# Kernel tuning notes

Hardware: AMD Instinct MI355X
Metric: run time of the kernel (lower is better)

The kernel has to match this reference:

```python
import jax, jax.numpy as jnp
import numpy as np

B, T, XD, ZD, H = 1024, 1000, 8, 8, 256


def setup_inputs() -> dict:
    key = jax.random.key(0)
    ks = jax.random.split(key, 10)
    # monotonically increasing time grid, identical per batch element: [B, T, 1]
    t = jnp.broadcast_to(jnp.linspace(0.0, 10.0, T, dtype=jnp.float32)[None, :, None], (B, T, 1))
    x = jax.random.normal(ks[0], (B, T, XD), jnp.float32)
    z = jax.random.normal(ks[1], (B, T, ZD), jnp.float32)
    event_t = jax.random.uniform(ks[2], (B, 1), jnp.float32, 3.0, 7.0)
    z_jump = jax.random.normal(ks[3], (B, ZD), jnp.float32)
    in_dim = 3 * (XD + ZD)

    def lin(k, fan_in, fan_out):
        return jax.random.normal(k, (fan_in, fan_out), jnp.float32) * (1.0 / np.sqrt(fan_in))

    W1 = lin(ks[4], in_dim, H); b1 = jnp.zeros((H,), jnp.float32)
    W2 = lin(ks[5], H, H);     b2 = jnp.zeros((H,), jnp.float32)
    W3 = lin(ks[6], H, H);     b3 = jnp.zeros((H,), jnp.float32)
    W4 = lin(ks[7], H, XD);    b4 = jnp.zeros((XD,), jnp.float32)
    return dict(t=t, x=x, z=z, event_t=event_t, z_jump=z_jump,
                W1=W1, b1=b1, W2=W2, b2=b2, W3=W3, b3=b3, W4=W4, b4=b4)


def reference(t, x, z, event_t, z_jump, W1, b1, W2, b2, W3, b3, W4, b4):
    # all_initial = cat(x[:,0], z[:,0]) : [B, XD+ZD]
    all_initial = jnp.concatenate([x[:, 0], z[:, 0]], axis=-1)

    def de_func(x_cur, z_eff):
        xtzt = jnp.concatenate([x_cur, z_eff], axis=-1)                      # [B, XD+ZD]
        inp = jnp.concatenate([all_initial, xtzt - all_initial, xtzt], -1)   # [B, 3*(XD+ZD)]
        h = jax.nn.elu(inp @ W1 + b1)
        h = jax.nn.elu(h @ W2 + b2)
        h = jax.nn.elu(h @ W3 + b3)
        return h @ W4 + b4                                                   # [B, XD]

    t_seq = jnp.moveaxis(t, 1, 0)   # [T, B, 1]
    z_seq = jnp.moveaxis(z, 1, 0)   # [T, B, ZD]
    dt = t_seq[1:] - t_seq[:-1]     # [T-1, B, 1]

    def step(x_cur, step_in):
        t_i, dt_i, z_i = step_in
        # event: once t passes event_t, exogenous z jumps to z_jump
        z_eff = jnp.where(t_i >= event_t, z_jump, z_i)
        x_next = x_cur + dt_i * de_func(x_cur, z_eff)  # explicit Euler step
        return x_next, x_next

    x0 = x[:, 0]  # initial condition [B, XD]
    _, xs = jax.lax.scan(step, x0, (t_seq[:-1], dt, z_seq[:-1]))
    sol = jnp.concatenate([x0[None], xs], axis=0)  # [T, B, XD]
    return jnp.moveaxis(sol, 0, 1)                 # [B, T, XD]
```

## Files before the change

kernel.cpp:

```cpp
#include <hip/hip_runtime.h>
#include <cstdint>
#include <cstddef>

typedef __bf16 bf16x8 __attribute__((ext_vector_type(8)));
typedef float f32x4 __attribute__((ext_vector_type(4)));

#define HD 256
#define TLEN 1000
#define NSTEP 999

#define W1R_OFF 0
#define W2R_OFF 16384
#define W3R_OFF 81920
#define W4R_OFF 147456
#define WS_ELEMS 151552

__device__ __forceinline__ void wg_barrier() {
  asm volatile("s_waitcnt lgkmcnt(0)\n\ts_barrier" ::: "memory");
}

__global__ void prep_weights(const float* __restrict__ W1, const float* __restrict__ b1,
                             const float* __restrict__ W2, const float* __restrict__ W3,
                             const float* __restrict__ W4, __bf16* __restrict__ ws) {
  int tid = blockIdx.x * blockDim.x + threadIdx.x;
  if (tid >= WS_ELEMS) return;
  float val = 0.0f;
  if (tid < W2R_OFF) {
    int t = tid;
    int j = t & 7, lane = (t >> 3) & 63, tt = (t >> 9) & 1, kb = (t >> 10) & 1, w = (t >> 11) & 7;
    int k = kb * 32 + ((lane >> 4) * 8) + j;
    int n = w * 32 + tt * 16 + (lane & 15);
    if (k < 48) val = W1[k * HD + n];
    else if (k == 48) val = b1[n];
  } else if (tid < W3R_OFF) {
    int t = tid - W2R_OFF;
    int j = t & 7, lane = (t >> 3) & 63, tt = (t >> 9) & 1, kb = (t >> 10) & 7, w = (t >> 13) & 7;
    int k = kb * 32 + ((lane >> 4) * 8) + j;
    int n = w * 32 + tt * 16 + (lane & 15);
    val = W2[k * HD + n];
  } else if (tid < W4R_OFF) {
    int t = tid - W3R_OFF;
    int j = t & 7, lane = (t >> 3) & 63, tt = (t >> 9) & 1, kb = (t >> 10) & 7, w = (t >> 13) & 7;
    int k = kb * 32 + ((lane >> 4) * 8) + j;
    int n = w * 32 + tt * 16 + (lane & 15);
    val = W3[k * HD + n];
  } else {
    int t = tid - W4R_OFF;
    int j = t & 7, lane = (t >> 3) & 63, kb = (t >> 9) & 7;
    int k = kb * 32 + ((lane >> 4) * 8) + j;
    int n = lane & 15;
    val = (n < 8) ? W4[k * 8 + n] : 0.0f;
  }
  ws[tid] = (__bf16)val;
}

__global__ __launch_bounds__(512, 2) void ode_main(
    const float* __restrict__ t_g, const float* __restrict__ x_g,
    const float* __restrict__ z_g, const float* __restrict__ ev_g,
    const float* __restrict__ zj_g, const float* __restrict__ b2_g,
    const float* __restrict__ b3_g, const float* __restrict__ b4_g,
    const __bf16* __restrict__ ws, float* __restrict__ out) {
  __shared__ __align__(16) __bf16 h_a[16 * 264];
  __shared__ __align__(16) __bf16 h_b[16 * 264];
  __shared__ __align__(16) float p4[8 * 16 * 8];
  __shared__ __align__(16) float x_cur[16 * 12];
  __shared__ __align__(16) float z_eff[16 * 12];
  __shared__ __align__(16) float x0s[16 * 12];
  __shared__ __align__(16) float z0s[16 * 12];
  __shared__ __align__(16) float zjs[16 * 12];
  __shared__ float evs[16];

  const int tid  = threadIdx.x;
  const int lane = tid & 63;
  const int wid  = tid >> 6;
  const int bcol = lane & 15;
  const int q    = lane >> 4;
  const int b0   = blockIdx.x * 8;

  if (tid < 128) {
    int m = tid >> 3, d = tid & 7;
    if (m < 8) {
      size_t gb = (size_t)(b0 + m);
      float x0 = x_g[gb * (TLEN * 8) + d];
      float z0 = z_g[gb * (TLEN * 8) + d];
      x0s[m * 12 + d] = x0;
      z0s[m * 12 + d] = z0;
      x_cur[m * 12 + d] = x0;
      zjs[m * 12 + d] = zj_g[gb * 8 + d];
      out[gb * (TLEN * 8) + d] = x0;
      if (d == 0) evs[m] = ev_g[gb];
    } else {
      x0s[m * 12 + d] = 0.f;
      z0s[m * 12 + d] = 0.f;
      x_cur[m * 12 + d] = 0.f;
      zjs[m * 12 + d] = 0.f;
      if (d == 0) evs[m] = 0.f;
    }
  }
  __syncthreads();

  if (tid < 128) {
    int m = tid >> 3, d = tid & 7;
    float t0 = t_g[0];
    z_eff[m * 12 + d] = (t0 >= evs[m]) ? zjs[m * 12 + d] : z0s[m * 12 + d];
  }

  const bf16x8* wsv = (const bf16x8*)ws;
  bf16x8 w1f[2][2], w2f[8][2], w3f[8][2];
#pragma unroll
  for (int kb = 0; kb < 2; ++kb)
#pragma unroll
    for (int tt = 0; tt < 2; ++tt)
      w1f[kb][tt] = wsv[(W1R_OFF / 8) + ((wid * 2 + kb) * 2 + tt) * 64 + lane];
#pragma unroll
  for (int kb = 0; kb < 8; ++kb)
#pragma unroll
    for (int tt = 0; tt < 2; ++tt) {
      w2f[kb][tt] = wsv[(W2R_OFF / 8) + ((wid * 8 + kb) * 2 + tt) * 64 + lane];
      w3f[kb][tt] = wsv[(W3R_OFF / 8) + ((wid * 8 + kb) * 2 + tt) * 64 + lane];
    }
  bf16x8 w4f = wsv[(W4R_OFF / 8) + wid * 64 + lane];

  f32x4 b2v[2], b3v[2];
#pragma unroll
  for (int tt = 0; tt < 2; ++tt) {
    int n0 = wid * 32 + tt * 16 + q * 4;
    b2v[tt] = *(const f32x4*)(b2_g + n0);
    b3v[tt] = *(const f32x4*)(b3_g + n0);
  }
  float b4l = (tid < 64) ? b4_g[tid & 7] : 0.0f;

  const int m1 = lane >> 2;
  const int d0 = (lane & 3) * 2;
  float2 zjf = make_float2(0.f, 0.f);
  float ev1 = 0.f;
  const bool zprod = (wid == 2) && (lane < 32);
  if (zprod) {
    zjf.x = zjs[m1 * 12 + d0];
    zjf.y = zjs[m1 * 12 + d0 + 1];
    ev1 = evs[m1];
  }

  f32x4 sub0, sub1;
  bf16x8 a0c;
  {
    const float* base = ((q & 1) ? z0s : x0s) + bcol * 12;
    f32x4 r0 = *(const f32x4*)(base);
    f32x4 r1 = *(const f32x4*)(base + 4);
    sub0 = r0; sub1 = r1;
#pragma unroll
    for (int e = 0; e < 4; ++e) { a0c[e] = (__bf16)r0[e]; a0c[e + 4] = (__bf16)r1[e]; }
  }
  bf16x8 zf;
#pragma unroll
  for (int e = 0; e < 8; ++e) zf[e] = (__bf16)0.f;
  bf16x8 k48f = zf;
  k48f[0] = (__bf16)1.0f;

  __syncthreads();

  float tc = t_g[0];

  auto layer = [&](const __bf16* src, __bf16* dst, const bf16x8 (*wf)[2], const f32x4* bv) {
    bf16x8 bfr[8];
    const bf16x8* hp = (const bf16x8*)src;
#pragma unroll
    for (int kb = 0; kb < 8; ++kb) bfr[kb] = hp[bcol * 33 + kb * 4 + q];
#pragma unroll
    for (int tt = 0; tt < 2; ++tt) {
      f32x4 c = bv[tt];
#pragma unroll
      for (int kb = 0; kb < 8; ++kb)
        c = __builtin_amdgcn_mfma_f32_16x16x32_bf16(wf[kb][tt], bfr[kb], c, 0, 0, 0);
      union { __bf16 h4[4]; unsigned long long u; } pk;
#pragma unroll
      for (int e = 0; e < 4; ++e) {
        float v = c[e];
        v = (v > 0.f) ? v : (__expf(v) - 1.0f);
        pk.h4[e] = (__bf16)v;
      }
      *(unsigned long long*)(dst + bcol * 264 + wid * 32 + tt * 16 + q * 4) = pk.u;
    }
  };

#pragma unroll 1
  for (int i = 0; i < NSTEP; ++i) {
    float tn = t_g[i + 1];
    float2 zpre = make_float2(0.f, 0.f);
    if (zprod)
      zpre = *(const float2*)(z_g + ((size_t)(b0 + m1) * TLEN + (i + 1)) * 8 + d0);

    {
      const float* rp = ((q & 1) ? z_eff : x_cur) + bcol * 12;
      f32x4 r0 = *(const f32x4*)(rp);
      f32x4 r1 = *(const f32x4*)(rp + 4);
      bf16x8 f0, f1;
      if (q < 2) {
        f0 = a0c;
#pragma unroll
        for (int e = 0; e < 4; ++e) { f1[e] = (__bf16)r0[e]; f1[e + 4] = (__bf16)r1[e]; }
      } else {
#pragma unroll
        for (int e = 0; e < 4; ++e) {
          f0[e] = (__bf16)(r0[e] - sub0[e]);
          f0[e + 4] = (__bf16)(r1[e] - sub1[e]);
        }
        f1 = (q == 2) ? k48f : zf;
      }
#pragma unroll
      for (int tt = 0; tt < 2; ++tt) {
        f32x4 c = {0.f, 0.f, 0.f, 0.f};
        c = __builtin_amdgcn_mfma_f32_16x16x32_bf16(w1f[0][tt], f0, c, 0, 0, 0);
        c = __builtin_amdgcn_mfma_f32_16x16x32_bf16(w1f[1][tt], f1, c, 0, 0, 0);
        union { __bf16 h4[4]; unsigned long long u; } pk;
#pragma unroll
        for (int e = 0; e < 4; ++e) {
          float v = c[e];
          v = (v > 0.f) ? v : (__expf(v) - 1.0f);
          pk.h4[e] = (__bf16)v;
        }
        *(unsigned long long*)(h_a + bcol * 264 + wid * 32 + tt * 16 + q * 4) = pk.u;
      }
    }
    wg_barrier();
    layer(h_a, h_b, w2f, b2v);
    wg_barrier();
    layer(h_b, h_a, w3f, b3v);

    {
      const bf16x8* hp = (const bf16x8*)h_a;
      bf16x8 h4 = hp[bcol * 33 + wid * 4 + q];
      f32x4 c = {0.f, 0.f, 0.f, 0.f};
      c = __builtin_amdgcn_mfma_f32_16x16x32_bf16(w4f, h4, c, 0, 0, 0);
      if (q < 2)
        *(f32x4*)(p4 + wid * 128 + bcol * 8 + q * 4) = c;
    }
    wg_barrier();

    float dt = tn - tc;
    if (tid < 64) {
      int m = tid >> 3, d = tid & 7;
      float s = b4l;
#pragma unroll
      for (int j = 0; j < 8; ++j) s += p4[j * 128 + m * 8 + d];
      float xn = x_cur[m * 12 + d] + dt * s;
      x_cur[m * 12 + d] = xn;
      out[(size_t)(b0 + m) * (TLEN * 8) + (size_t)(i + 1) * 8 + d] = xn;
    } else if (zprod) {
      bool jmp = (tn >= ev1);
      float2 zev = make_float2(jmp ? zjf.x : zpre.x, jmp ? zjf.y : zpre.y);
      *(float2*)(z_eff + m1 * 12 + d0) = zev;
    }
    tc = tn;
    wg_barrier();
  }
}

extern "C" void kernel_launch(void* const* d_in, const int* in_sizes, int n_in,
                              void* d_out, int out_size, void* d_ws, size_t ws_size,
                              hipStream_t stream) {
  const float* t  = (const float*)d_in[0];
  const float* x  = (const float*)d_in[1];
  const float* z  = (const float*)d_in[2];
  const float* ev = (const float*)d_in[3];
  const float* zj = (const float*)d_in[4];
  const float* W1 = (const float*)d_in[5];
  const float* b1 = (const float*)d_in[6];
  const float* W2 = (const float*)d_in[7];
  const float* b2 = (const float*)d_in[8];
  const float* W3 = (const float*)d_in[9];
  const float* b3 = (const float*)d_in[10];
  const float* W4 = (const float*)d_in[11];
  const float* b4 = (const float*)d_in[12];
  __bf16* ws = (__bf16*)d_ws;
  float* out = (float*)d_out;

  prep_weights<<<592, 256, 0, stream>>>(W1, b1, W2, W3, W4, ws);
  ode_main<<<128, 512, 0, stream>>>(t, x, z, ev, zj, b2, b3, b4, ws, out);
}
```

Before: 1.764 ms.

## Fold constant W1 terms into per-block init and compute output layer redundantly per wave

Rewrites layer 1 algebraically: the all_initial and bias contributions are precomputed once into a per-wave accumulator, and the per-step input shrinks to a single K=32 MFMA per tile using combined W1 rows. Every wave now computes the full layer-4 output itself, with a full K reduction held in registers, so the p4 shared reduction is gone. The x and z state lives in registers, which removes one barrier per step. Layer 2/3 accumulation is split into two independent MFMA chains to shorten the dependency chain. In exchange, each wave does redundant layer-4 MFMAs, holds extra weight registers, and uses a third LDS buffer.

New measurement: 2.024 ms. 1.15x slower.

```diff
diff --git a/kernel.cpp b/kernel.cpp
--- a/kernel.cpp
+++ b/kernel.cpp
@@ -9,7 +9,8 @@
 #define TLEN 1000
 #define NSTEP 999
 
-#define W1R_OFF 0
+#define W1X_OFF 0
+#define W1C_OFF 8192
 #define W2R_OFF 16384
 #define W3R_OFF 81920
 #define W4R_OFF 147456
@@ -25,13 +26,28 @@
   int tid = blockIdx.x * blockDim.x + threadIdx.x;
   if (tid >= WS_ELEMS) return;
   float val = 0.0f;
-  if (tid < W2R_OFF) {
+  if (tid < W1C_OFF) {
     int t = tid;
-    int j = t & 7, lane = (t >> 3) & 63, tt = (t >> 9) & 1, kb = (t >> 10) & 1, w = (t >> 11) & 7;
-    int k = kb * 32 + ((lane >> 4) * 8) + j;
-    int n = w * 32 + tt * 16 + (lane & 15);
-    if (k < 48) val = W1[k * HD + n];
-    else if (k == 48) val = b1[n];
+    int j = t & 7, lane = (t >> 3) & 63, tt = (t >> 9) & 1, w = (t >> 10) & 7;
+    int q = lane >> 4;
+    int n = w * 32 + tt * 16 + (lane & 15);
+    if (j < 4) {
+      int d = q * 4 + j;
+      if (q < 2) val = W1[(16 + d) * HD + n] + W1[(32 + d) * HD + n];
+      else { int dz = d - 8; val = W1[(24 + dz) * HD + n] + W1[(40 + dz) * HD + n]; }
+    }
+  } else if (tid < W2R_OFF) {
+    int t = tid - W1C_OFF;
+    int j = t & 7, lane = (t >> 3) & 63, tt = (t >> 9) & 1, w = (t >> 10) & 7;
+    int q = lane >> 4;
+    int n = w * 32 + tt * 16 + (lane & 15);
+    if (j < 4) {
+      int d = q * 4 + j;
+      if (q < 2) val = W1[d * HD + n] - W1[(16 + d) * HD + n];
+      else { int dz = d - 8; val = W1[(8 + dz) * HD + n] - W1[(24 + dz) * HD + n]; }
+    } else if (q == 0 && j == 4) {
+      val = b1[n];
+    }
   } else if (tid < W3R_OFF) {
     int t = tid - W2R_OFF;
     int j = t & 7, lane = (t >> 3) & 63, tt = (t >> 9) & 1, kb = (t >> 10) & 7, w = (t >> 13) & 7;
@@ -39,7 +55,8 @@
     int n = w * 32 + tt * 16 + (lane & 15);
     val = W2[k * HD + n];
   } else if (tid < W4R_OFF) {
-    int t = tid - W3R_OFF;
+    int t = tid - W4R_OFF + (W4R_OFF - W3R_OFF);
+    t = tid - W3R_OFF;
     int j = t & 7, lane = (t >> 3) & 63, tt = (t >> 9) & 1, kb = (t >> 10) & 7, w = (t >> 13) & 7;
     int k = kb * 32 + ((lane >> 4) * 8) + j;
     int n = w * 32 + tt * 16 + (lane & 15);
@@ -60,15 +77,9 @@
     const float* __restrict__ zj_g, const float* __restrict__ b2_g,
     const float* __restrict__ b3_g, const float* __restrict__ b4_g,
     const __bf16* __restrict__ ws, float* __restrict__ out) {
-  __shared__ __align__(16) __bf16 h_a[16 * 264];
-  __shared__ __align__(16) __bf16 h_b[16 * 264];
-  __shared__ __align__(16) float p4[8 * 16 * 8];
-  __shared__ __align__(16) float x_cur[16 * 12];
-  __shared__ __align__(16) float z_eff[16 * 12];
-  __shared__ __align__(16) float x0s[16 * 12];
-  __shared__ __align__(16) float z0s[16 * 12];
-  __shared__ __align__(16) float zjs[16 * 12];
-  __shared__ float evs[16];
+  __shared__ __align__(16) __bf16 hA[16 * 264];
+  __shared__ __align__(16) __bf16 hB[16 * 264];
+  __shared__ __align__(16) __bf16 hC[16 * 264];
 
   const int tid  = threadIdx.x;
   const int lane = tid & 63;
@@ -76,50 +87,23 @@
   const int bcol = lane & 15;
   const int q    = lane >> 4;
   const int b0   = blockIdx.x * 8;
-
-  if (tid < 128) {
-    int m = tid >> 3, d = tid & 7;
-    if (m < 8) {
-      size_t gb = (size_t)(b0 + m);
-      float x0 = x_g[gb * (TLEN * 8) + d];
-      float z0 = z_g[gb * (TLEN * 8) + d];
-      x0s[m * 12 + d] = x0;
-      z0s[m * 12 + d] = z0;
-      x_cur[m * 12 + d] = x0;
-      zjs[m * 12 + d] = zj_g[gb * 8 + d];
-      out[gb * (TLEN * 8) + d] = x0;
-      if (d == 0) evs[m] = ev_g[gb];
-    } else {
-      x0s[m * 12 + d] = 0.f;
-      z0s[m * 12 + d] = 0.f;
-      x_cur[m * 12 + d] = 0.f;
-      zjs[m * 12 + d] = 0.f;
-      if (d == 0) evs[m] = 0.f;
-    }
-  }
-  __syncthreads();
-
-  if (tid < 128) {
-    int m = tid >> 3, d = tid & 7;
-    float t0 = t_g[0];
-    z_eff[m * 12 + d] = (t0 >= evs[m]) ? zjs[m * 12 + d] : z0s[m * 12 + d];
-  }
+  const bool live = bcol < 8;
+  const size_t gb = (size_t)(b0 + (live ? bcol : 0));
 
   const bf16x8* wsv = (const bf16x8*)ws;
-  bf16x8 w1f[2][2], w2f[8][2], w3f[8][2];
-#pragma unroll
-  for (int kb = 0; kb < 2; ++kb)
-#pragma unroll
-    for (int tt = 0; tt < 2; ++tt)
-      w1f[kb][tt] = wsv[(W1R_OFF / 8) + ((wid * 2 + kb) * 2 + tt) * 64 + lane];
-#pragma unroll
-  for (int kb = 0; kb < 8; ++kb)
+  bf16x8 w1f[2], w2f[8][2], w3f[8][2], w4f[8];
+#pragma unroll
+  for (int tt = 0; tt < 2; ++tt)
+    w1f[tt] = wsv[(W1X_OFF / 8) + (wid * 2 + tt) * 64 + lane];
+#pragma unroll
+  for (int kb = 0; kb < 8; ++kb) {
 #pragma unroll
     for (int tt = 0; tt < 2; ++tt) {
       w2f[kb][tt] = wsv[(W2R_OFF / 8) + ((wid * 8 + kb) * 2 + tt) * 64 + lane];
       w3f[kb][tt] = wsv[(W3R_OFF / 8) + ((wid * 8 + kb) * 2 + tt) * 64 + lane];
     }
-  bf16x8 w4f = wsv[(W4R_OFF / 8) + wid * 64 + lane];
+    w4f[kb] = wsv[(W4R_OFF / 8) + kb * 64 + lane];
+  }
 
   f32x4 b2v[2], b3v[2];
 #pragma unroll
@@ -128,38 +112,62 @@
     b2v[tt] = *(const f32x4*)(b2_g + n0);
     b3v[tt] = *(const f32x4*)(b3_g + n0);
   }
-  float b4l = (tid < 64) ? b4_g[tid & 7] : 0.0f;
-
-  const int m1 = lane >> 2;
-  const int d0 = (lane & 3) * 2;
-  float2 zjf = make_float2(0.f, 0.f);
+  f32x4 b4v = {0.f, 0.f, 0.f, 0.f};
+  if (q < 2) b4v = *(const f32x4*)(b4_g + q * 4);
+
+  f32x4 init4 = {0.f, 0.f, 0.f, 0.f};
+  if (live) {
+    const float* p = (q < 2) ? (x_g + gb * (TLEN * 8) + q * 4)
+                             : (z_g + gb * (TLEN * 8) + (q - 2) * 4);
+    init4 = *(const f32x4*)p;
+  }
   float ev1 = 0.f;
-  const bool zprod = (wid == 2) && (lane < 32);
-  if (zprod) {
-    zjf.x = zjs[m1 * 12 + d0];
-    zjf.y = zjs[m1 * 12 + d0 + 1];
-    ev1 = evs[m1];
-  }
-
-  f32x4 sub0, sub1;
-  bf16x8 a0c;
+  bf16x8 zjh;
+#pragma unroll
+  for (int e = 0; e < 8; ++e) zjh[e] = (__bf16)0.f;
+  if (q >= 2 && live) {
+    ev1 = ev_g[gb];
+    f32x4 zj4 = *(const f32x4*)(zj_g + gb * 8 + (q - 2) * 4);
+#pragma unroll
+    for (int e = 0; e < 4; ++e) zjh[e] = (__bf16)zj4[e];
+  }
+
+  float t0 = t_g[0];
+
+  f32x4 c1init[2];
   {
-    const float* base = ((q & 1) ? z0s : x0s) + bcol * 12;
-    f32x4 r0 = *(const f32x4*)(base);
-    f32x4 r1 = *(const f32x4*)(base + 4);
-    sub0 = r0; sub1 = r1;
-#pragma unroll
-    for (int e = 0; e < 4; ++e) { a0c[e] = (__bf16)r0[e]; a0c[e + 4] = (__bf16)r1[e]; }
-  }
-  bf16x8 zf;
-#pragma unroll
-  for (int e = 0; e < 8; ++e) zf[e] = (__bf16)0.f;
-  bf16x8 k48f = zf;
-  k48f[0] = (__bf16)1.0f;
-
-  __syncthreads();
-
-  float tc = t_g[0];
+    bf16x8 cb;
+#pragma unroll
+    for (int e = 0; e < 8; ++e) cb[e] = (__bf16)0.f;
+#pragma unroll
+    for (int e = 0; e < 4; ++e) cb[e] = (__bf16)init4[e];
+    if (q == 0) cb[4] = (__bf16)1.0f;
+#pragma unroll
+    for (int tt = 0; tt < 2; ++tt) {
+      bf16x8 w1cf = wsv[(W1C_OFF / 8) + (wid * 2 + tt) * 64 + lane];
+      f32x4 z4 = {0.f, 0.f, 0.f, 0.f};
+      c1init[tt] = __builtin_amdgcn_mfma_f32_16x16x32_bf16(w1cf, cb, z4, 0, 0, 0);
+    }
+  }
+
+  f32x4 xc4 = {0.f, 0.f, 0.f, 0.f};
+  if (q < 2) xc4 = init4;
+  bf16x8 myfrag;
+#pragma unroll
+  for (int e = 0; e < 8; ++e) myfrag[e] = (__bf16)0.f;
+  if (q < 2) {
+#pragma unroll
+    for (int e = 0; e < 4; ++e) myfrag[e] = (__bf16)init4[e];
+  } else {
+    bool jmp0 = (t0 >= ev1);
+#pragma unroll
+    for (int e = 0; e < 4; ++e) myfrag[e] = jmp0 ? zjh[e] : (__bf16)init4[e];
+  }
+
+  if (wid == 0 && q < 2 && live)
+    *(f32x4*)(out + gb * (TLEN * 8) + q * 4) = init4;
+
+  float tc = t0;
 
   auto layer = [&](const __bf16* src, __bf16* dst, const bf16x8 (*wf)[2], const f32x4* bv) {
     bf16x8 bfr[8];
@@ -168,10 +176,35 @@
     for (int kb = 0; kb < 8; ++kb) bfr[kb] = hp[bcol * 33 + kb * 4 + q];
 #pragma unroll
     for (int tt = 0; tt < 2; ++tt) {
-      f32x4 c = bv[tt];
-#pragma unroll
-      for (int kb = 0; kb < 8; ++kb)
-        c = __builtin_amdgcn_mfma_f32_16x16x32_bf16(wf[kb][tt], bfr[kb], c, 0, 0, 0);
+      f32x4 c0 = bv[tt];
+      f32x4 c1 = {0.f, 0.f, 0.f, 0.f};
+#pragma unroll
+      for (int kb = 0; kb < 4; ++kb)
+        c0 = __builtin_amdgcn_mfma_f32_16x16x32_bf16(wf[kb][tt], bfr[kb], c0, 0, 0, 0);
+#pragma unroll
+      for (int kb = 4; kb < 8; ++kb)
+        c1 = __builtin_amdgcn_mfma_f32_16x16x32_bf16(wf[kb][tt], bfr[kb], c1, 0, 0, 0);
+      union { __bf16 h4[4]; unsigned long long u; } pk;
+#pragma unroll
+      for (int e = 0; e < 4; ++e) {
+        float v = c0[e] + c1[e];
+        v = (v > 0.f) ? v : (__expf(v) - 1.0f);
+        pk.h4[e] = (__bf16)v;
+      }
+      *(unsigned long long*)(dst + bcol * 264 + wid * 32 + tt * 16 + q * 4) = pk.u;
+    }
+  };
+
+#pragma unroll 1
+  for (int i = 0; i < NSTEP; ++i) {
+    float tn = t_g[i + 1];
+    f32x4 zp4 = {0.f, 0.f, 0.f, 0.f};
+    if (q >= 2 && live)
+      zp4 = *(const f32x4*)(z_g + (gb * TLEN + (size_t)(i + 1)) * 8 + (q - 2) * 4);
+
+#pragma unroll
+    for (int tt = 0; tt < 2; ++tt) {
+      f32x4 c = __builtin_amdgcn_mfma_f32_16x16x32_bf16(w1f[tt], myfrag, c1init[tt], 0, 0, 0);
       union { __bf16 h4[4]; unsigned long long u; } pk;
 #pragma unroll
       for (int e = 0; e < 4; ++e) {
@@ -179,80 +212,43 @@
         v = (v > 0.f) ? v : (__expf(v) - 1.0f);
         pk.h4[e] = (__bf16)v;
       }
-      *(unsigned long long*)(dst + bcol * 264 + wid * 32 + tt * 16 + q * 4) = pk.u;
-    }
-  };
-
-#pragma unroll 1
-  for (int i = 0; i < NSTEP; ++i) {
-    float tn = t_g[i + 1];
-    float2 zpre = make_float2(0.f, 0.f);
-    if (zprod)
-      zpre = *(const float2*)(z_g + ((size_t)(b0 + m1) * TLEN + (i + 1)) * 8 + d0);
+      *(unsigned long long*)(hA + bcol * 264 + wid * 32 + tt * 16 + q * 4) = pk.u;
+    }
+    wg_barrier();
+    layer(hA, hB, w2f, b2v);
+    wg_barrier();
+    layer(hB, hC, w3f, b3v);
+    wg_barrier();
 
     {
-      const float* rp = ((q & 1) ? z_eff : x_cur) + bcol * 12;
-      f32x4 r0 = *(const f32x4*)(rp);
-      f32x4 r1 = *(const f32x4*)(rp + 4);
-      bf16x8 f0, f1;
+      const bf16x8* hp = (const bf16x8*)hC;
+      bf16x8 br[8];
+#pragma unroll
+      for (int kb = 0; kb < 8; ++kb) br[kb] = hp[bcol * 33 + kb * 4 + q];
+      f32x4 c0 = {0.f, 0.f, 0.f, 0.f}, c1 = {0.f, 0.f, 0.f, 0.f};
+#pragma unroll
+      for (int kb = 0; kb < 4; ++kb)
+        c0 = __builtin_amdgcn_mfma_f32_16x16x32_bf16(w4f[kb], br[kb], c0, 0, 0, 0);
+#pragma unroll
+      for (int kb = 4; kb < 8; ++kb)
+        c1 = __builtin_amdgcn_mfma_f32_16x16x32_bf16(w4f[kb], br[kb], c1, 0, 0, 0);
+      float dt = tn - tc;
+      f32x4 xn;
+#pragma unroll
+      for (int e = 0; e < 4; ++e) xn[e] = xc4[e] + dt * (c0[e] + c1[e] + b4v[e]);
+      xc4 = xn;
+      if (wid == 0 && q < 2 && live)
+        *(f32x4*)(out + gb * (TLEN * 8) + (size_t)(i + 1) * 8 + q * 4) = xn;
       if (q < 2) {
-        f0 = a0c;
-#pragma unroll
-        for (int e = 0; e < 4; ++e) { f1[e] = (__bf16)r0[e]; f1[e + 4] = (__bf16)r1[e]; }
+#pragma unroll
+        for (int e = 0; e < 4; ++e) myfrag[e] = (__bf16)xn[e];
       } else {
-#pragma unroll
-        for (int e = 0; e < 4; ++e) {
-          f0[e] = (__bf16)(r0[e] - sub0[e]);
-          f0[e + 4] = (__bf16)(r1[e] - sub1[e]);
-        }
-        f1 = (q == 2) ? k48f : zf;
+        bool jmp = (tn >= ev1);
+#pragma unroll
+        for (int e = 0; e < 4; ++e) myfrag[e] = jmp ? zjh[e] : (__bf16)zp4[e];
       }
-#pragma unroll
-      for (int tt = 0; tt < 2; ++tt) {
-        f32x4 c = {0.f, 0.f, 0.f, 0.f};
-        c = __builtin_amdgcn_mfma_f32_16x16x32_bf16(w1f[0][tt], f0, c, 0, 0, 0);
-        c = __builtin_amdgcn_mfma_f32_16x16x32_bf16(w1f[1][tt], f1, c, 0, 0, 0);
-        union { __bf16 h4[4]; unsigned long long u; } pk;
-#pragma unroll
-        for (int e = 0; e < 4; ++e) {
-          float v = c[e];
-          v = (v > 0.f) ? v : (__expf(v) - 1.0f);
-          pk.h4[e] = (__bf16)v;
-        }
-        *(unsigned long long*)(h_a + bcol * 264 + wid * 32 + tt * 16 + q * 4) = pk.u;
-      }
-    }
-    wg_barrier();
-    layer(h_a, h_b, w2f, b2v);
-    wg_barrier();
-    layer(h_b, h_a, w3f, b3v);
-
-    {
-      const bf16x8* hp = (const bf16x8*)h_a;
-      bf16x8 h4 = hp[bcol * 33 + wid * 4 + q];
-      f32x4 c = {0.f, 0.f, 0.f, 0.f};
-      c = __builtin_amdgcn_mfma_f32_16x16x32_bf16(w4f, h4, c, 0, 0, 0);
-      if (q < 2)
-        *(f32x4*)(p4 + wid * 128 + bcol * 8 + q * 4) = c;
-    }
-    wg_barrier();
-
-    float dt = tn - tc;
-    if (tid < 64) {
-      int m = tid >> 3, d = tid & 7;
-      float s = b4l;
-#pragma unroll
-      for (int j = 0; j < 8; ++j) s += p4[j * 128 + m * 8 + d];
-      float xn = x_cur[m * 12 + d] + dt * s;
-      x_cur[m * 12 + d] = xn;
-      out[(size_t)(b0 + m) * (TLEN * 8) + (size_t)(i + 1) * 8 + d] = xn;
-    } else if (zprod) {
-      bool jmp = (tn >= ev1);
-      float2 zev = make_float2(jmp ? zjf.x : zpre.x, jmp ? zjf.y : zpre.y);
-      *(float2*)(z_eff + m1 * 12 + d0) = zev;
     }
     tc = tn;
-    wg_barrier();
   }
 }
 
```
